# Kernel optimization log

Measured on AMD Instinct MI355X. Metric: run time of the kernel, lower is better.

The kernel has to match this reference:

```python
import jax, jax.numpy as jnp
import numpy as np

JOBS, FEAT, BATCH = 150, 15, 32
H1, D1 = 3, 64          # layer1: 3 heads x 64, concatenated -> 192
H2, D2 = 3, 128         # layer2: 3 heads x 128, averaged -> 128
GNN_OUT = D2 + FEAT     # 143 (gnn output concat with raw node features)
HID = 64


def _gat_layer(h_in, W, a_src, a_dst):
    # h_in: [N, F]; W: [F, H, D]; a_src/a_dst: [H, D]
    h = jnp.einsum('nf,fhd->nhd', h_in, W)                 # [N, H, D]
    s = jnp.einsum('nhd,hd->nh', h, a_src)                 # target score
    t = jnp.einsum('nhd,hd->nh', h, a_dst)                 # source score
    e = jax.nn.leaky_relu(s[:, None, :] + t[None, :, :], 0.2)   # [N, N, H]
    alpha = jax.nn.softmax(e, axis=1)                      # softmax over sources j
    return jnp.einsum('ijh,jhd->ihd', alpha, h)            # [N, H, D]


def setup_inputs() -> dict:
    key = jax.random.key(0)
    ks = jax.random.split(key, 12)
    sc = 0.1
    return {
        'real_obs': jax.random.normal(ks[0], (BATCH, JOBS, FEAT), jnp.float32),
        'action_mask': jnp.ones((BATCH, JOBS + 1), jnp.float32),
        'W1': jax.random.normal(ks[1], (FEAT, H1, D1), jnp.float32) * sc,
        'a_src1': jax.random.normal(ks[2], (H1, D1), jnp.float32) * sc,
        'a_dst1': jax.random.normal(ks[3], (H1, D1), jnp.float32) * sc,
        'W2': jax.random.normal(ks[4], (H1 * D1, H2, D2), jnp.float32) * sc,
        'a_src2': jax.random.normal(ks[5], (H2, D2), jnp.float32) * sc,
        'a_dst2': jax.random.normal(ks[6], (H2, D2), jnp.float32) * sc,
        'P1': jax.random.normal(ks[7], (GNN_OUT, 2 * HID), jnp.float32) * sc,
        'b1': jnp.zeros((2 * HID,), jnp.float32),
        'P2': jax.random.normal(ks[8], (2 * HID, HID), jnp.float32) * sc,
        'b2': jnp.zeros((HID,), jnp.float32),
    }


def reference(real_obs, action_mask, W1, a_src1, a_dst1, W2, a_src2, a_dst2, P1, b1, P2, b2):
    B = real_obs.shape[0]
    flat = real_obs.reshape(B * JOBS, FEAT)                        # N=4800 nodes, fully connected
    h1 = _gat_layer(flat, W1, a_src1, a_dst1)                      # [N, 3, 64]
    h1 = jax.nn.elu(h1.reshape(h1.shape[0], -1))                   # concat heads -> [N, 192]
    h2 = _gat_layer(h1, W2, a_src2, a_dst2).mean(axis=1)           # avg heads -> [N, 128]
    g = jnp.concatenate([h2, flat], axis=-1)                       # [N, 143]
    f = jax.nn.relu(g @ P1 + b1)
    f = jax.nn.relu(f @ P2 + b2)                                   # [N, 64]
    features = f.reshape(B, JOBS, HID).mean(axis=1)                # mean pool -> [B, 64]
    return features, action_mask
```

## Files before the change

### kernel.cpp

```cpp
#include <hip/hip_runtime.h>
#include <hip/hip_bf16.h>

typedef __attribute__((ext_vector_type(8))) short short8;
typedef __attribute__((ext_vector_type(4))) float f32x4;

#define NN 4800
#define NN1 4801
#define NC 240
#define CL 20
#define KLEN 600

__device__ __forceinline__ short bf16rne(float x) {
    unsigned u = __float_as_uint(x);
    u = (u + 0x7FFFu + ((u >> 16) & 1u)) >> 16;
    return (short)u;
}
__device__ __forceinline__ unsigned fkey(float f) {
    unsigned i = __float_as_uint(f);
    return (i & 0x80000000u) ? ~i : (i | 0x80000000u);
}

__global__ __launch_bounds__(256) void prep(
    const float* __restrict__ flat, const float* __restrict__ amask,
    const float* __restrict__ W1, const float* __restrict__ as1, const float* __restrict__ ad1,
    const float* __restrict__ W2, const float* __restrict__ P1, const float* __restrict__ P2,
    float* __restrict__ h1, float* __restrict__ s1, float* __restrict__ t1,
    short* __restrict__ W2T, short* __restrict__ P1T, short* __restrict__ P2T,
    float* __restrict__ out) {
    const int gtid = blockIdx.x * 256 + threadIdx.x;
    const int GT = 1200 * 256;
    for (int x = gtid; x < 109280; x += GT) {
        if (x < 73728) {
            int n = x / 192, k = x % 192;
            W2T[x] = bf16rne(W2[k * 384 + n]);
        } else if (x < 94208) {
            int z = x - 73728; int n = z / 160, k = z % 160;
            P1T[z] = bf16rne(k < 143 ? P1[k * 128 + n] : 0.f);
        } else if (x < 102400) {
            int z = x - 94208; int n = z / 128, k = z % 128;
            P2T[z] = bf16rne(P2[k * 64 + n]);
        } else if (x < 107232) {
            int m = x - 102400;
            out[2048 + m] = amask[m];
        } else {
            out[x - 107232] = 0.f;
        }
    }
    const int lane = threadIdx.x & 63;
    const int gw = (gtid >> 6);
    for (int task = gw; task < 3 * NN; task += (GT >> 6)) {
        int h = task / NN, i = task % NN;
        int col = h * 64 + lane;
        const float* fr = flat + i * 15;
        float hv = 0.f;
#pragma unroll
        for (int f = 0; f < 15; ++f) hv += fr[f] * W1[f * 192 + col];
        h1[i * 192 + col] = hv;
        float ps = hv * as1[col], pt = hv * ad1[col];
#pragma unroll
        for (int off = 32; off; off >>= 1) { ps += __shfl_xor(ps, off); pt += __shfl_xor(pt, off); }
        if (lane == 0) { s1[h * NN + i] = ps; t1[h * NN + i] = pt; }
    }
}

__global__ __launch_bounds__(256) void krank(const float* __restrict__ s, const float* __restrict__ t,
                                             int* __restrict__ partial) {
    __shared__ __align__(16) unsigned long long ts[KLEN];
    const int h = blockIdx.y, kc = blockIdx.z;
    const float* tp = t + h * NN + kc * KLEN;
    for (int k = threadIdx.x; k < KLEN; k += 256)
        ts[k] = ((unsigned long long)fkey(tp[k]) << 32) | (unsigned)k;
    __syncthreads();
    int q = blockIdx.x * 256 + threadIdx.x;
    if (q >= 2 * NN) return;
    unsigned long long uq;
    if (q < NN) {
        int tb = q - kc * KLEN;
        int tbc = tb < 0 ? 0 : (tb > KLEN ? KLEN : tb);
        uq = ((unsigned long long)fkey(t[h * NN + q]) << 32) | (unsigned)tbc;
    } else {
        uq = ((unsigned long long)fkey(-s[h * NN + q - NN]) << 32) | (unsigned)KLEN;
    }
    int cnt = 0;
#pragma unroll 4
    for (int k = 0; k < KLEN; k += 2) {
        ulonglong2 v = *(const ulonglong2*)&ts[k];
        cnt += (v.x < uq);
        cnt += (v.y < uq);
    }
    partial[(kc * 3 + h) * (2 * NN) + q] = cnt;
}

__global__ __launch_bounds__(256) void ksc1(const float* __restrict__ t, const int* __restrict__ partial,
                                            int* __restrict__ inv, float* __restrict__ e1s,
                                            float* __restrict__ e2s, int* __restrict__ rks) {
    int idx = blockIdx.x * 256 + threadIdx.x;
    if (idx >= 3 * 2 * NN) return;
    int h = idx / (2 * NN), q = idx % (2 * NN);
    int sum = 0;
#pragma unroll
    for (int kc = 0; kc < 8; ++kc) sum += partial[(kc * 3 + h) * (2 * NN) + q];
    if (q < NN) {
        float tv = t[h * NN + q];
        inv[h * NN + sum] = q;
        e1s[h * NN + sum] = __expf(tv);
        e2s[h * NN + sum] = __expf(0.2f * tv);
    } else {
        rks[h * NN + q - NN] = sum;
    }
}

template <int Dd, int HD, int PACK>
__global__ __launch_bounds__(256) void phA(const float* __restrict__ hsrc, const int* __restrict__ inv,
                                           const float* __restrict__ e1s, const float* __restrict__ e2s,
                                           float* __restrict__ T1, float* __restrict__ T2) {
    __shared__ int inv_l[PACK * CL];
    __shared__ float w1s[PACK * CL], w2s[PACK * CL];
    const int h = blockIdx.y, tid = threadIdx.x;
    const int base = blockIdx.x * (PACK * CL);
    if (tid < PACK * CL) {
        inv_l[tid] = inv[h * NN + base + tid];
        w1s[tid] = e1s[h * NN + base + tid];
        w2s[tid] = e2s[h * NN + base + tid];
    }
    __syncthreads();
    const int sub = tid / Dd, d = tid % Dd;
    const int c = blockIdx.x * PACK + sub;
    float a1 = 0.f, a2 = 0.f;
#pragma unroll
    for (int p = 0; p < CL; ++p) {
        int j = inv_l[sub * CL + p];
        float hv = hsrc[(size_t)j * HD + h * Dd + d];
        a1 += w1s[sub * CL + p] * hv;
        a2 += w2s[sub * CL + p] * hv;
    }
    T1[(h * NC + c) * Dd + d] = a1;
    T2[(h * NC + c) * Dd + d] = a2;
}

template <int Dd>
__global__ __launch_bounds__(256) void phBden(const float* __restrict__ T1, const float* __restrict__ T2,
                                              const float* __restrict__ e1s, const float* __restrict__ e2s,
                                              float* __restrict__ O1, float* __restrict__ O2,
                                              float* __restrict__ DenS1, float* __restrict__ DenP2) {
    constexpr int G = Dd / 32;
    constexpr int NSCAN = 6 * G;
    __shared__ __align__(16) float smem[9608];
    const int tid = threadIdx.x;
    if (blockIdx.x < NSCAN) {
        float (*ls)[32] = (float(*)[32])smem;
        double* sbd = (double*)(smem + 7680);
        const int b = blockIdx.x;
        const int h = b % 3, rest = b / 3, dir = rest & 1, dg = rest >> 1;
        const float* T = dir ? T2 : T1;
        for (int idx = tid; idx < NC * 32; idx += 256) {
            int c = idx >> 5, dl = idx & 31;
            ls[c][dl] = T[(h * NC + c) * Dd + dg * 32 + dl];
        }
        __syncthreads();
        const int seg = tid >> 5, dl = tid & 31;
        double ssum = 0.0;
#pragma unroll
        for (int k = 0; k < 30; ++k) ssum += (double)ls[seg * 30 + k][dl];
        sbd[seg * 32 + dl] = ssum;
        __syncthreads();
        double off = 0.0;
        if (dir == 0) { for (int k = seg + 1; k < 8; ++k) off += sbd[k * 32 + dl]; }
        else          { for (int k = 0; k < seg; ++k)     off += sbd[k * 32 + dl]; }
        float* O = dir ? O2 : O1;
        const int d = dg * 32 + dl;
        double r = off;
        if (dir == 0) {
#pragma unroll
            for (int k = 29; k >= 0; --k) {
                int c = seg * 30 + k;
                O[(h * NC + c) * Dd + d] = (float)r;
                r += (double)ls[c][dl];
            }
        } else {
#pragma unroll
            for (int k = 0; k < 30; ++k) {
                int c = seg * 30 + k;
                O[(h * NC + c) * Dd + d] = (float)r;
                r += (double)ls[c][dl];
            }
        }
        return;
    }
    const int h = blockIdx.x - NSCAN;
    float* l1 = smem;
    float* l2 = smem + NN;
    float* wsum = smem + 9600;
    for (int k = tid; k < NN; k += 256) { l1[k] = e1s[h * NN + k]; l2[k] = e2s[h * NN + k]; }
    __syncthreads();
    const int p0 = tid * 19;
    const int cnt = (p0 < NN) ? ((NN - p0 < 19) ? NN - p0 : 19) : 0;
    float sA = 0.f, sB = 0.f;
    for (int k = 0; k < cnt; ++k) { sA += l1[p0 + k]; sB += l2[p0 + k]; }
    float iA = sA, iB = sB;
    const int lane = tid & 63, w = tid >> 6;
#pragma unroll
    for (int d2 = 1; d2 < 64; d2 <<= 1) {
        float uA = __shfl_up(iA, d2), uB = __shfl_up(iB, d2);
        if (lane >= d2) { iA += uA; iB += uB; }
    }
    if (lane == 63) { wsum[w] = iA; wsum[4 + w] = iB; }
    __syncthreads();
    float baseA = 0.f, baseB = 0.f;
    for (int k = 0; k < w; ++k) { baseA += wsum[k]; baseB += wsum[4 + k]; }
    float TA = wsum[0] + wsum[1] + wsum[2] + wsum[3];
    float rA = baseA + iA - sA;
    float rB = baseB + iB - sB;
    for (int k = 0; k < cnt; ++k) {
        int p = p0 + k;
        DenS1[h * NN1 + p] = TA - rA;
        DenP2[h * NN1 + p] = rB;
        rA += l1[p]; rB += l2[p];
    }
    if (tid == 255) {
        DenS1[h * NN1 + NN] = 0.f;
        DenP2[h * NN1 + NN] = wsum[4] + wsum[5] + wsum[6] + wsum[7];
    }
}

template <int Dd, int HD, int PACK>
__global__ __launch_bounds__(256) void phC(const float* __restrict__ hsrc, const int* __restrict__ inv,
                                           const float* __restrict__ e1s, const float* __restrict__ e2s,
                                           const float* __restrict__ O1, const float* __restrict__ O2,
                                           float* __restrict__ Suf1, float* __restrict__ Pre2) {
    __shared__ int inv_l[PACK * CL];
    __shared__ float w1s[PACK * CL], w2s[PACK * CL];
    const int h = blockIdx.y, tid = threadIdx.x;
    const int base = blockIdx.x * (PACK * CL);
    if (tid < PACK * CL) {
        inv_l[tid] = inv[h * NN + base + tid];
        w1s[tid] = e1s[h * NN + base + tid];
        w2s[tid] = e2s[h * NN + base + tid];
    }
    __syncthreads();
    const int sub = tid / Dd, d = tid % Dd;
    const int c = blockIdx.x * PACK + sub;
    float hv[CL];
#pragma unroll
    for (int p = 0; p < CL; ++p) {
        int j = inv_l[sub * CL + p];
        hv[p] = hsrc[(size_t)j * HD + h * Dd + d];
    }
    float r2 = O2[(h * NC + c) * Dd + d];
#pragma unroll
    for (int p = 0; p < CL; ++p) {
        int pp = c * CL + p;
        Pre2[((size_t)(h * NN1) + pp) * Dd + d] = r2;
        r2 += w2s[sub * CL + p] * hv[p];
    }
    if (c == NC - 1) {
        Pre2[((size_t)(h * NN1) + NN) * Dd + d] = r2;
        Suf1[((size_t)(h * NN1) + NN) * Dd + d] = 0.f;
    }
    float r1 = O1[(h * NC + c) * Dd + d];
#pragma unroll
    for (int p = CL - 1; p >= 0; --p) {
        int pp = c * CL + p;
        r1 += w1s[sub * CL + p] * hv[p];
        Suf1[((size_t)(h * NN1) + pp) * Dd + d] = r1;
    }
}

__global__ __launch_bounds__(256) void kout1(const float* __restrict__ s1, const int* __restrict__ rks1,
                                             const float* __restrict__ Suf1, const float* __restrict__ Pre2,
                                             const float* __restrict__ DenS1, const float* __restrict__ DenP2,
                                             short* __restrict__ h1abf,
                                             float* __restrict__ s2, float* __restrict__ t2) {
    const int gtid = blockIdx.x * 256 + threadIdx.x;
    if (gtid < 3 * NN) { s2[gtid] = 0.f; t2[gtid] = 0.f; }
    for (int x = gtid; x < NN * 192; x += 900 * 256) {
        int i = x / 192, cc = x % 192, h = cc >> 6, d = cc & 63;
        float sv = s1[h * NN + i];
        float a = __expf(sv), b = __expf(0.2f * sv);
        int r = rks1[h * NN + i];
        size_t bp = ((size_t)(h * NN1) + r) * 64 + d;
        float num = a * Suf1[bp] + b * Pre2[bp];
        float den = a * DenS1[h * NN1 + r] + b * DenP2[h * NN1 + r];
        float v = num / den;
        v = v > 0.f ? v : (__expf(v) - 1.f);
        h1abf[x] = bf16rne(v);
    }
}

__global__ __launch_bounds__(256) void gemm1(const short* __restrict__ A, const short* __restrict__ W2T,
                                             const float* __restrict__ as2, const float* __restrict__ ad2,
                                             float* __restrict__ h2, float* __restrict__ s2,
                                             float* __restrict__ t2) {
    const int mb = blockIdx.x, nb = blockIdx.y, tid = threadIdx.x;
    const int lane = tid & 63, w = tid >> 6, q = lane >> 4, mr = lane & 15;
    const int m = mb * 64 + w * 16 + mr, n0 = nb * 64, hh = nb >> 1;
    f32x4 acc[4];
#pragma unroll
    for (int n = 0; n < 4; ++n) acc[n] = (f32x4){0.f, 0.f, 0.f, 0.f};
#pragma unroll
    for (int k0 = 0; k0 < 192; k0 += 32) {
        short8 af = *(const short8*)(A + (size_t)m * 192 + k0 + q * 8);
#pragma unroll
        for (int n = 0; n < 4; ++n) {
            short8 bf = *(const short8*)(W2T + (size_t)(n0 + n * 16 + mr) * 192 + k0 + q * 8);
            acc[n] = __builtin_amdgcn_mfma_f32_16x16x32_bf16(af, bf, acc[n], 0, 0, 0);
        }
    }
    float pse[4] = {0.f, 0.f, 0.f, 0.f}, pte[4] = {0.f, 0.f, 0.f, 0.f};
#pragma unroll
    for (int n = 0; n < 4; ++n) {
        int col = n0 + n * 16 + mr;
        float va = as2[col], vd = ad2[col];
#pragma unroll
        for (int r = 0; r < 4; ++r) {
            int row = mb * 64 + w * 16 + q * 4 + r;
            float v = acc[n][r];
            h2[(size_t)row * 384 + col] = v;
            pse[r] += v * va;
            pte[r] += v * vd;
        }
    }
#pragma unroll
    for (int off = 1; off < 16; off <<= 1) {
#pragma unroll
        for (int r = 0; r < 4; ++r) {
            pse[r] += __shfl_xor(pse[r], off);
            pte[r] += __shfl_xor(pte[r], off);
// ... 66 lines not shown
    }
    __syncthreads();
    f32x4 a2 = (f32x4){0.f, 0.f, 0.f, 0.f};
#pragma unroll
    for (int k0 = 0; k0 < 128; k0 += 32) {
        short8 af = *(const short8*)&f1[mr][k0 + q * 8];
        short8 bf = *(const short8*)(P2T + (size_t)(w * 16 + mr) * 128 + k0 + q * 8);
        a2 = __builtin_amdgcn_mfma_f32_16x16x32_bf16(af, bf, a2, 0, 0, 0);
    }
    float* f2f = (float*)&g[0][0];
    {
        int col = w * 16 + mr;
        float bv = b2[col];
#pragma unroll
        for (int r = 0; r < 4; ++r) {
            int row = q * 4 + r;
            f2f[row * 65 + col] = fmaxf(a2[r] + bv, 0.f);
        }
    }
    __syncthreads();
    if (tid < 64) {
        int d = tid;
        int b0 = (mb * 16) / 150;
        int bend = (mb * 16 + 15) / 150;
        float sa = 0.f, sb = 0.f;
        for (int row = 0; row < 16; ++row) {
            float v = f2f[row * 65 + d];
            int b = (mb * 16 + row) / 150;
            if (b == b0) sa += v; else sb += v;
        }
        atomicAdd(&out[b0 * 64 + d], sa * (1.f / 150.f));
        if (bend != b0) atomicAdd(&out[bend * 64 + d], sb * (1.f / 150.f));
    }
}

extern "C" void kernel_launch(void* const* d_in, const int* in_sizes, int n_in,
                              void* d_out, int out_size, void* d_ws, size_t ws_size,
                              hipStream_t stream) {
    const float* flat   = (const float*)d_in[0];
    const float* amask  = (const float*)d_in[1];
    const float* W1     = (const float*)d_in[2];
    const float* a_src1 = (const float*)d_in[3];
    const float* a_dst1 = (const float*)d_in[4];
    const float* W2     = (const float*)d_in[5];
    const float* a_src2 = (const float*)d_in[6];
    const float* a_dst2 = (const float*)d_in[7];
    const float* P1     = (const float*)d_in[8];
    const float* b1     = (const float*)d_in[9];
    const float* P2     = (const float*)d_in[10];
    const float* b2     = (const float*)d_in[11];
    float* out = (float*)d_out;

    char* wsb = (char*)d_ws;
    int*   partial = (int*)  (wsb + 0);
    float* s1      = (float*)(wsb + 921600);
    float* t1      = (float*)(wsb + 979200);
    float* s2      = (float*)(wsb + 1036800);
    float* t2      = (float*)(wsb + 1094400);
    int*   rks1    = (int*)  (wsb + 1152000);
    int*   rks2    = (int*)  (wsb + 1209600);
    float* h1      = (float*)(wsb + 1267200);
    int*   inv     = (int*)  (wsb + 4953600);
    float* e1s     = (float*)(wsb + 5011200);
    float* e2s     = (float*)(wsb + 5068800);
    float* DenS1   = (float*)(wsb + 5126400);
    float* DenP2   = (float*)(wsb + 5184064);
    float* Tot1    = (float*)(wsb + 5241728);
    float* Tot2    = (float*)(wsb + 5610368);
    float* Off1    = (float*)(wsb + 5979008);
    float* Off2    = (float*)(wsb + 6347648);
    float* Suf1    = (float*)(wsb + 6716288);
    float* Pre2    = (float*)(wsb + 14090624);
    float* h2      = (float*)(wsb + 21464960);
    short* h1abf   = (short*)(wsb + 28837760);
    short* W2T     = (short*)(wsb + 30680960);
    short* P1T     = (short*)(wsb + 30828416);
    short* P2T     = (short*)(wsb + 30869376);

    prep<<<1200, 256, 0, stream>>>(flat, amask, W1, a_src1, a_dst1, W2, P1, P2,
                                   h1, s1, t1, W2T, P1T, P2T, out);
    krank<<<dim3(38, 3, 8), 256, 0, stream>>>(s1, t1, partial);
    ksc1<<<113, 256, 0, stream>>>(t1, partial, inv, e1s, e2s, rks1);
    phA<64, 192, 4><<<dim3(60, 3), 256, 0, stream>>>(h1, inv, e1s, e2s, Tot1, Tot2);
    phBden<64><<<15, 256, 0, stream>>>(Tot1, Tot2, e1s, e2s, Off1, Off2, DenS1, DenP2);
    phC<64, 192, 4><<<dim3(60, 3), 256, 0, stream>>>(h1, inv, e1s, e2s, Off1, Off2, Suf1, Pre2);
    kout1<<<900, 256, 0, stream>>>(s1, rks1, Suf1, Pre2, DenS1, DenP2, h1abf, s2, t2);
    gemm1<<<dim3(75, 6), 256, 0, stream>>>(h1abf, W2T, a_src2, a_dst2, h2, s2, t2);
    krank<<<dim3(38, 3, 8), 256, 0, stream>>>(s2, t2, partial);
    ksc1<<<113, 256, 0, stream>>>(t2, partial, inv, e1s, e2s, rks2);
    phA<128, 384, 2><<<dim3(120, 3), 256, 0, stream>>>(h2, inv, e1s, e2s, Tot1, Tot2);
    phBden<128><<<27, 256, 0, stream>>>(Tot1, Tot2, e1s, e2s, Off1, Off2, DenS1, DenP2);
    phC<128, 384, 2><<<dim3(120, 3), 256, 0, stream>>>(h2, inv, e1s, e2s, Off1, Off2, Suf1, Pre2);
    tail2<<<300, 256, 0, stream>>>(s2, rks2, Suf1, Pre2, DenS1, DenP2, flat, P1T, P2T, b1, b2, out);
}
```

Before: 183.0 us.

## Fuse rank reduction into atomics and fold scan kernels into neighbors

The rank-count kernel now accumulates its partial counts with a packed atomic that also counts finished chunks. The last arriving block performs the scatter, which removes the separate reduction kernel and its partial buffer pass. The denominator prefix scan moves into an extra block of the cluster-aggregation kernel. The per-cluster offset scan is recomputed redundantly inside the suffix/prefix kernel from the cluster totals. Together this removes two launches per layer, at the cost of atomic contention and redundant serial double-precision summation over up to 240 clusters per block.

Measured after the change: 241.6 us. 32.0% more time.

```diff
diff --git a/kernel.cpp b/kernel.cpp
--- a/kernel.cpp
+++ b/kernel.cpp
@@ -1,8 +1,8 @@
 #include <hip/hip_runtime.h>
-#include <hip/hip_bf16.h>
 
 typedef __attribute__((ext_vector_type(8))) short short8;
 typedef __attribute__((ext_vector_type(4))) float f32x4;
+typedef unsigned long long ull;
 
 #define NN 4800
 #define NN1 4801
@@ -26,10 +26,10 @@
     const float* __restrict__ W2, const float* __restrict__ P1, const float* __restrict__ P2,
     float* __restrict__ h1, float* __restrict__ s1, float* __restrict__ t1,
     short* __restrict__ W2T, short* __restrict__ P1T, short* __restrict__ P2T,
-    float* __restrict__ out) {
+    float* __restrict__ out, int* __restrict__ partial) {
     const int gtid = blockIdx.x * 256 + threadIdx.x;
     const int GT = 1200 * 256;
-    for (int x = gtid; x < 109280; x += GT) {
+    for (int x = gtid; x < 138080; x += GT) {
         if (x < 73728) {
             int n = x / 192, k = x % 192;
             W2T[x] = bf16rne(W2[k * 384 + n]);
@@ -42,8 +42,10 @@
         } else if (x < 107232) {
             int m = x - 102400;
             out[2048 + m] = amask[m];
+        } else if (x < 109280) {
+            out[x - 107232] = 0.f;
         } else {
-            out[x - 107232] = 0.f;
+            partial[x - 109280] = 0;
         }
     }
     const int lane = threadIdx.x & 63;
@@ -63,23 +65,25 @@
     }
 }
 
-__global__ __launch_bounds__(256) void krank(const float* __restrict__ s, const float* __restrict__ t,
-                                             int* __restrict__ partial) {
-    __shared__ __align__(16) unsigned long long ts[KLEN];
+__global__ __launch_bounds__(256) void krks(const float* __restrict__ s, const float* __restrict__ t,
+                                            int* __restrict__ acc, int* __restrict__ inv,
+                                            float* __restrict__ e1s, float* __restrict__ e2s,
+                                            int* __restrict__ rks) {
+    __shared__ __align__(16) ull ts[KLEN];
     const int h = blockIdx.y, kc = blockIdx.z;
     const float* tp = t + h * NN + kc * KLEN;
     for (int k = threadIdx.x; k < KLEN; k += 256)
-        ts[k] = ((unsigned long long)fkey(tp[k]) << 32) | (unsigned)k;
+        ts[k] = ((ull)fkey(tp[k]) << 32) | (unsigned)k;
     __syncthreads();
     int q = blockIdx.x * 256 + threadIdx.x;
     if (q >= 2 * NN) return;
-    unsigned long long uq;
+    ull uq;
     if (q < NN) {
         int tb = q - kc * KLEN;
         int tbc = tb < 0 ? 0 : (tb > KLEN ? KLEN : tb);
-        uq = ((unsigned long long)fkey(t[h * NN + q]) << 32) | (unsigned)tbc;
+        uq = ((ull)fkey(t[h * NN + q]) << 32) | (unsigned)tbc;
     } else {
-        uq = ((unsigned long long)fkey(-s[h * NN + q - NN]) << 32) | (unsigned)KLEN;
+        uq = ((ull)fkey(-s[h * NN + q - NN]) << 32) | (unsigned)KLEN;
     }
     int cnt = 0;
 #pragma unroll 4
@@ -88,36 +92,65 @@
         cnt += (v.x < uq);
         cnt += (v.y < uq);
     }
-    partial[(kc * 3 + h) * (2 * NN) + q] = cnt;
-}
-
-__global__ __launch_bounds__(256) void ksc1(const float* __restrict__ t, const int* __restrict__ partial,
-                                            int* __restrict__ inv, float* __restrict__ e1s,
-                                            float* __restrict__ e2s, int* __restrict__ rks) {
-    int idx = blockIdx.x * 256 + threadIdx.x;
-    if (idx >= 3 * 2 * NN) return;
-    int h = idx / (2 * NN), q = idx % (2 * NN);
-    int sum = 0;
-#pragma unroll
-    for (int kc = 0; kc < 8; ++kc) sum += partial[(kc * 3 + h) * (2 * NN) + q];
-    if (q < NN) {
-        float tv = t[h * NN + q];
-        inv[h * NN + sum] = q;
-        e1s[h * NN + sum] = __expf(tv);
-        e2s[h * NN + sum] = __expf(0.2f * tv);
-    } else {
-        rks[h * NN + q - NN] = sum;
+    unsigned ret = atomicAdd((unsigned*)&acc[h * 2 * NN + q], (unsigned)cnt | (1u << 24));
+    if ((ret >> 24) == 7u) {
+        int sum = (int)((ret & 0xFFFFFFu) + (unsigned)cnt);
+        if (q < NN) {
+            float tv = t[h * NN + q];
+            inv[h * NN + sum] = q;
+            e1s[h * NN + sum] = __expf(tv);
+            e2s[h * NN + sum] = __expf(0.2f * tv);
+        } else {
+            rks[h * NN + q - NN] = sum;
+        }
     }
 }
 
 template <int Dd, int HD, int PACK>
-__global__ __launch_bounds__(256) void phA(const float* __restrict__ hsrc, const int* __restrict__ inv,
-                                           const float* __restrict__ e1s, const float* __restrict__ e2s,
-                                           float* __restrict__ T1, float* __restrict__ T2) {
+__global__ __launch_bounds__(256) void phAden(const float* __restrict__ hsrc, const int* __restrict__ inv,
+                                              const float* __restrict__ e1s, const float* __restrict__ e2s,
+                                              float* __restrict__ T1, float* __restrict__ T2,
+                                              float* __restrict__ DenS1, float* __restrict__ DenP2) {
+    constexpr int NB = NC / PACK;
     __shared__ int inv_l[PACK * CL];
     __shared__ float w1s[PACK * CL], w2s[PACK * CL];
+    __shared__ float wsum[8];
     const int h = blockIdx.y, tid = threadIdx.x;
-    const int base = blockIdx.x * (PACK * CL);
+    if (blockIdx.x == NB) {
+        const float* l1 = e1s + h * NN;
+        const float* l2 = e2s + h * NN;
+        const int p0 = tid * 19;
+        const int cnt = (p0 < NN) ? ((NN - p0 < 19) ? NN - p0 : 19) : 0;
+        float sA = 0.f, sB = 0.f;
+        for (int k = 0; k < cnt; ++k) { sA += l1[p0 + k]; sB += l2[p0 + k]; }
+        float iA = sA, iB = sB;
+        const int lane = tid & 63, w = tid >> 6;
+#pragma unroll
+        for (int d2 = 1; d2 < 64; d2 <<= 1) {
+            float uA = __shfl_up(iA, d2), uB = __shfl_up(iB, d2);
+            if (lane >= d2) { iA += uA; iB += uB; }
+        }
+        if (lane == 63) { wsum[w] = iA; wsum[4 + w] = iB; }
+        __syncthreads();
+        float baseA = 0.f, baseB = 0.f;
+        for (int k = 0; k < w; ++k) { baseA += wsum[k]; baseB += wsum[4 + k]; }
+        float TA = wsum[0] + wsum[1] + wsum[2] + wsum[3];
+        float rA = baseA + iA - sA;
+        float rB = baseB + iB - sB;
+        for (int k = 0; k < cnt; ++k) {
+            int p = p0 + k;
+            DenS1[h * NN1 + p] = TA - rA;
+            DenP2[h * NN1 + p] = rB;
+            rA += l1[p]; rB += l2[p];
+        }
+        if (tid == 255) {
+            DenS1[h * NN1 + NN] = 0.f;
+            DenP2[h * NN1 + NN] = wsum[4] + wsum[5] + wsum[6] + wsum[7];
+        }
+        return;
+    }
+    const int cb = blockIdx.x;
+    const int base = cb * (PACK * CL);
     if (tid < PACK * CL) {
         inv_l[tid] = inv[h * NN + base + tid];
         w1s[tid] = e1s[h * NN + base + tid];
@@ -125,7 +158,7 @@
     }
     __syncthreads();
     const int sub = tid / Dd, d = tid % Dd;
-    const int c = blockIdx.x * PACK + sub;
+    const int c = cb * PACK + sub;
     float a1 = 0.f, a2 = 0.f;
 #pragma unroll
     for (int p = 0; p < CL; ++p) {
@@ -138,115 +171,69 @@
     T2[(h * NC + c) * Dd + d] = a2;
 }
 
-template <int Dd>
-__global__ __launch_bounds__(256) void phBden(const float* __restrict__ T1, const float* __restrict__ T2,
-                                              const float* __restrict__ e1s, const float* __restrict__ e2s,
-                                              float* __restrict__ O1, float* __restrict__ O2,
-                                              float* __restrict__ DenS1, float* __restrict__ DenP2) {
-    constexpr int G = Dd / 32;
-    constexpr int NSCAN = 6 * G;
-    __shared__ __align__(16) float smem[9608];
-    const int tid = threadIdx.x;
-    if (blockIdx.x < NSCAN) {
-        float (*ls)[32] = (float(*)[32])smem;
-        double* sbd = (double*)(smem + 7680);
-        const int b = blockIdx.x;
-        const int h = b % 3, rest = b / 3, dir = rest & 1, dg = rest >> 1;
-        const float* T = dir ? T2 : T1;
-        for (int idx = tid; idx < NC * 32; idx += 256) {
-            int c = idx >> 5, dl = idx & 31;
-            ls[c][dl] = T[(h * NC + c) * Dd + dg * 32 + dl];
-        }
-        __syncthreads();
-        const int seg = tid >> 5, dl = tid & 31;
-        double ssum = 0.0;
-#pragma unroll
-        for (int k = 0; k < 30; ++k) ssum += (double)ls[seg * 30 + k][dl];
-        sbd[seg * 32 + dl] = ssum;
-        __syncthreads();
-        double off = 0.0;
-        if (dir == 0) { for (int k = seg + 1; k < 8; ++k) off += sbd[k * 32 + dl]; }
-        else          { for (int k = 0; k < seg; ++k)     off += sbd[k * 32 + dl]; }
-        float* O = dir ? O2 : O1;
-        const int d = dg * 32 + dl;
-        double r = off;
-        if (dir == 0) {
-#pragma unroll
-            for (int k = 29; k >= 0; --k) {
-                int c = seg * 30 + k;
-                O[(h * NC + c) * Dd + d] = (float)r;
-                r += (double)ls[c][dl];
-            }
-        } else {
-#pragma unroll
-            for (int k = 0; k < 30; ++k) {
-                int c = seg * 30 + k;
-                O[(h * NC + c) * Dd + d] = (float)r;
-                r += (double)ls[c][dl];
-            }
-        }
-        return;
-    }
-    const int h = blockIdx.x - NSCAN;
-    float* l1 = smem;
-    float* l2 = smem + NN;
-    float* wsum = smem + 9600;
-    for (int k = tid; k < NN; k += 256) { l1[k] = e1s[h * NN + k]; l2[k] = e2s[h * NN + k]; }
-    __syncthreads();
-    const int p0 = tid * 19;
-    const int cnt = (p0 < NN) ? ((NN - p0 < 19) ? NN - p0 : 19) : 0;
-    float sA = 0.f, sB = 0.f;
-    for (int k = 0; k < cnt; ++k) { sA += l1[p0 + k]; sB += l2[p0 + k]; }
-    float iA = sA, iB = sB;
-    const int lane = tid & 63, w = tid >> 6;
-#pragma unroll
-    for (int d2 = 1; d2 < 64; d2 <<= 1) {
-        float uA = __shfl_up(iA, d2), uB = __shfl_up(iB, d2);
-        if (lane >= d2) { iA += uA; iB += uB; }
-    }
-    if (lane == 63) { wsum[w] = iA; wsum[4 + w] = iB; }
-    __syncthreads();
-    float baseA = 0.f, baseB = 0.f;
-    for (int k = 0; k < w; ++k) { baseA += wsum[k]; baseB += wsum[4 + k]; }
-    float TA = wsum[0] + wsum[1] + wsum[2] + wsum[3];
-    float rA = baseA + iA - sA;
-    float rB = baseB + iB - sB;
-    for (int k = 0; k < cnt; ++k) {
-        int p = p0 + k;
-        DenS1[h * NN1 + p] = TA - rA;
-        DenP2[h * NN1 + p] = rB;
-        rA += l1[p]; rB += l2[p];
-    }
-    if (tid == 255) {
-        DenS1[h * NN1 + NN] = 0.f;
-        DenP2[h * NN1 + NN] = wsum[4] + wsum[5] + wsum[6] + wsum[7];
-    }
-}
-
 template <int Dd, int HD, int PACK>
-__global__ __launch_bounds__(256) void phC(const float* __restrict__ hsrc, const int* __restrict__ inv,
-                                           const float* __restrict__ e1s, const float* __restrict__ e2s,
-                                           const float* __restrict__ O1, const float* __restrict__ O2,
-                                           float* __restrict__ Suf1, float* __restrict__ Pre2) {
+__global__ __launch_bounds__(256) void phCs(const float* __restrict__ hsrc, const int* __restrict__ inv,
+                                            const float* __restrict__ e1s, const float* __restrict__ e2s,
+                                            const float* __restrict__ T1, const float* __restrict__ T2,
+                                            float* __restrict__ Suf1, float* __restrict__ Pre2) {
     __shared__ int inv_l[PACK * CL];
     __shared__ float w1s[PACK * CL], w2s[PACK * CL];
-    const int h = blockIdx.y, tid = threadIdx.x;
-    const int base = blockIdx.x * (PACK * CL);
+    __shared__ double o1d[Dd], o2d[Dd];
+    const int h = blockIdx.y, cb = blockIdx.x, tid = threadIdx.x;
+    const int base = cb * (PACK * CL);
     if (tid < PACK * CL) {
         inv_l[tid] = inv[h * NN + base + tid];
         w1s[tid] = e1s[h * NN + base + tid];
         w2s[tid] = e2s[h * NN + base + tid];
     }
-    __syncthreads();
     const int sub = tid / Dd, d = tid % Dd;
-    const int c = blockIdx.x * PACK + sub;
+    const int c = cb * PACK + sub;
+    const int cmin = cb * PACK, cmax = cb * PACK + PACK - 1;
+    double o1 = 0.0, o2 = 0.0;
+    if (sub == PACK - 1) {
+        double e0 = 0.0, e1 = 0.0;
+        int cc = c + 1;
+        for (; cc + 1 < NC; cc += 2) {
+            e0 += (double)T1[(h * NC + cc) * Dd + d];
+            e1 += (double)T1[(h * NC + cc + 1) * Dd + d];
+        }
+        if (cc < NC) e0 += (double)T1[(h * NC + cc) * Dd + d];
+        o1 = e0 + e1; o1d[d] = o1;
+    }
+    if (sub == 0) {
+        double e0 = 0.0, e1 = 0.0;
+        int cc = 0;
+        for (; cc + 1 < c; cc += 2) {
+            e0 += (double)T2[(h * NC + cc) * Dd + d];
+            e1 += (double)T2[(h * NC + cc + 1) * Dd + d];
+        }
+        if (cc < c) e0 += (double)T2[(h * NC + cc) * Dd + d];
+        o2 = e0 + e1; o2d[d] = o2;
+    }
+    __syncthreads();
+    if (sub != PACK - 1) {
+        o1 = o1d[d];
+#pragma unroll
+        for (int cc2 = 0; cc2 < PACK - 1; ++cc2) {
+            int cc = c + 1 + cc2;
+            if (cc <= cmax) o1 += (double)T1[(h * NC + cc) * Dd + d];
+        }
+    }
+    if (sub != 0) {
+        o2 = o2d[d];
+#pragma unroll
+        for (int cc2 = 0; cc2 < PACK - 1; ++cc2) {
+            int cc = cmin + cc2;
+            if (cc < c) o2 += (double)T2[(h * NC + cc) * Dd + d];
+        }
+    }
     float hv[CL];
 #pragma unroll
     for (int p = 0; p < CL; ++p) {
         int j = inv_l[sub * CL + p];
         hv[p] = hsrc[(size_t)j * HD + h * Dd + d];
     }
-    float r2 = O2[(h * NC + c) * Dd + d];
+    float r2 = (float)o2;
 #pragma unroll
     for (int p = 0; p < CL; ++p) {
         int pp = c * CL + p;
@@ -257,7 +244,7 @@
         Pre2[((size_t)(h * NN1) + NN) * Dd + d] = r2;
         Suf1[((size_t)(h * NN1) + NN) * Dd + d] = 0.f;
     }
-    float r1 = O1[(h * NC + c) * Dd + d];
+    float r1 = (float)o1;
 #pragma unroll
     for (int p = CL - 1; p >= 0; --p) {
         int pp = c * CL + p;
@@ -270,9 +257,11 @@
                                              const float* __restrict__ Suf1, const float* __restrict__ Pre2,
                                              const float* __restrict__ DenS1, const float* __restrict__ DenP2,
                                              short* __restrict__ h1abf,
-                                             float* __restrict__ s2, float* __restrict__ t2) {
+                                             float* __restrict__ s2, float* __restrict__ t2,
+                                             int* __restrict__ partial) {
     const int gtid = blockIdx.x * 256 + threadIdx.x;
     if (gtid < 3 * NN) { s2[gtid] = 0.f; t2[gtid] = 0.f; }
+    if (gtid < 3 * 2 * NN) partial[gtid] = 0;
     for (int x = gtid; x < NN * 192; x += 900 * 256) {
         int i = x / 192, cc = x % 192, h = cc >> 6, d = cc & 63;
         float sv = s1[h * NN + i];
@@ -460,8 +449,6 @@
     float* DenP2   = (float*)(wsb + 5184064);
     float* Tot1    = (float*)(wsb + 5241728);
     float* Tot2    = (float*)(wsb + 5610368);
-    float* Off1    = (float*)(wsb + 5979008);
-    float* Off2    = (float*)(wsb + 6347648);
     float* Suf1    = (float*)(wsb + 6716288);
     float* Pre2    = (float*)(wsb + 14090624);
     float* h2      = (float*)(wsb + 21464960);
@@ -471,18 +458,14 @@
     short* P2T     = (short*)(wsb + 30869376);
 
     prep<<<1200, 256, 0, stream>>>(flat, amask, W1, a_src1, a_dst1, W2, P1, P2,
-                                   h1, s1, t1, W2T, P1T, P2T, out);
-    krank<<<dim3(38, 3, 8), 256, 0, stream>>>(s1, t1, partial);
-    ksc1<<<113, 256, 0, stream>>>(t1, partial, inv, e1s, e2s, rks1);
-    phA<64, 192, 4><<<dim3(60, 3), 256, 0, stream>>>(h1, inv, e1s, e2s, Tot1, Tot2);
-    phBden<64><<<15, 256, 0, stream>>>(Tot1, Tot2, e1s, e2s, Off1, Off2, DenS1, DenP2);
-    phC<64, 192, 4><<<dim3(60, 3), 256, 0, stream>>>(h1, inv, e1s, e2s, Off1, Off2, Suf1, Pre2);
-    kout1<<<900, 256, 0, stream>>>(s1, rks1, Suf1, Pre2, DenS1, DenP2, h1abf, s2, t2);
+                                   h1, s1, t1, W2T, P1T, P2T, out, partial);
+    krks<<<dim3(38, 3, 8), 256, 0, stream>>>(s1, t1, partial, inv, e1s, e2s, rks1);
+    phAden<64, 192, 4><<<dim3(61, 3), 256, 0, stream>>>(h1, inv, e1s, e2s, Tot1, Tot2, DenS1, DenP2);
+    phCs<64, 192, 4><<<dim3(60, 3), 256, 0, stream>>>(h1, inv, e1s, e2s, Tot1, Tot2, Suf1, Pre2);
+    kout1<<<900, 256, 0, stream>>>(s1, rks1, Suf1, Pre2, DenS1, DenP2, h1abf, s2, t2, partial);
     gemm1<<<dim3(75, 6), 256, 0, stream>>>(h1abf, W2T, a_src2, a_dst2, h2, s2, t2);
-    krank<<<dim3(38, 3, 8), 256, 0, stream>>>(s2, t2, partial);
-    ksc1<<<113, 256, 0, stream>>>(t2, partial, inv, e1s, e2s, rks2);
-    phA<128, 384, 2><<<dim3(120, 3), 256, 0, stream>>>(h2, inv, e1s, e2s, Tot1, Tot2);
-    phBden<128><<<27, 256, 0, stream>>>(Tot1, Tot2, e1s, e2s, Off1, Off2, DenS1, DenP2);
-    phC<128, 384, 2><<<dim3(120, 3), 256, 0, stream>>>(h2, inv, e1s, e2s, Off1, Off2, Suf1, Pre2);
+    krks<<<dim3(38, 3, 8), 256, 0, stream>>>(s2, t2, partial, inv, e1s, e2s, rks2);
+    phAden<128, 384, 2><<<dim3(121, 3), 256, 0, stream>>>(h2, inv, e1s, e2s, Tot1, Tot2, DenS1, DenP2);
+    phCs<128, 384, 2><<<dim3(120, 3), 256, 0, stream>>>(h2, inv, e1s, e2s, Tot1, Tot2, Suf1, Pre2);
     tail2<<<300, 256, 0, stream>>>(s2, rks2, Suf1, Pre2, DenS1, DenP2, flat, P1T, P2T, b1, b2, out);
 }
```

## Replace brute-force rank counting with chunk bitonic sort plus binary search

Applied to the files above, without the earlier changes.

The old krank compared every query against all 600 keys of each of 8 chunks, then a separate kernel summed the partial counts and scattered the results. The new code bitonic-sorts each 600-key chunk in shared memory, padded to 1024. A fused kernel then binary-searches each sorted chunk and does the scatter directly, which cuts the comparison work from linear to logarithmic and removes one launch and the partial-count buffer. In exchange there are two small, serial-ish launches: the sort uses only 24 blocks with many syncthreads, and the search loop reloads shared memory 8 times per block.

Result: slower. 233.2 us (+27.4%).

```diff
diff --git a/kernel.cpp b/kernel.cpp
--- a/kernel.cpp
+++ b/kernel.cpp
@@ -1,8 +1,8 @@
 #include <hip/hip_runtime.h>
-#include <hip/hip_bf16.h>
 
 typedef __attribute__((ext_vector_type(8))) short short8;
 typedef __attribute__((ext_vector_type(4))) float f32x4;
+typedef unsigned long long ull;
 
 #define NN 4800
 #define NN1 4801
@@ -63,50 +63,64 @@
     }
 }
 
-__global__ __launch_bounds__(256) void krank(const float* __restrict__ s, const float* __restrict__ t,
-                                             int* __restrict__ partial) {
-    __shared__ __align__(16) unsigned long long ts[KLEN];
-    const int h = blockIdx.y, kc = blockIdx.z;
+__global__ __launch_bounds__(256) void sortk(const float* __restrict__ t, ull* __restrict__ sortedK) {
+    __shared__ ull ls[1024];
+    const int kc = blockIdx.x, h = blockIdx.y, tid = threadIdx.x;
     const float* tp = t + h * NN + kc * KLEN;
-    for (int k = threadIdx.x; k < KLEN; k += 256)
-        ts[k] = ((unsigned long long)fkey(tp[k]) << 32) | (unsigned)k;
-    __syncthreads();
-    int q = blockIdx.x * 256 + threadIdx.x;
-    if (q >= 2 * NN) return;
-    unsigned long long uq;
+    for (int i = tid; i < 1024; i += 256)
+        ls[i] = (i < KLEN) ? (((ull)fkey(tp[i]) << 32) | (unsigned)(kc * KLEN + i)) : ~0ull;
+    __syncthreads();
+    for (int k = 2; k <= 1024; k <<= 1) {
+        for (int j = k >> 1; j > 0; j >>= 1) {
+            for (int i = tid; i < 1024; i += 256) {
+                int p = i ^ j;
+                if (p > i) {
+                    ull a = ls[i], b = ls[p];
+                    bool up = ((i & k) == 0);
+                    if ((a > b) == up) { ls[i] = b; ls[p] = a; }
+                }
+            }
+            __syncthreads();
+        }
+    }
+    ull* dst = sortedK + (h * 8 + kc) * KLEN;
+    for (int i = tid; i < KLEN; i += 256) dst[i] = ls[i];
+}
+
+__global__ __launch_bounds__(256) void kranksc(const float* __restrict__ s, const float* __restrict__ t,
+                                               const ull* __restrict__ sortedK,
+                                               int* __restrict__ inv, float* __restrict__ e1s,
+                                               float* __restrict__ e2s, int* __restrict__ rks) {
+    __shared__ __align__(16) ull ts[KLEN];
+    const int h = blockIdx.y, tid = threadIdx.x;
+    const int q = blockIdx.x * 256 + tid;
+    const bool active = q < 2 * NN;
+    ull uq = 0; float tv = 0.f;
+    if (active) {
+        if (q < NN) { tv = t[h * NN + q]; uq = ((ull)fkey(tv) << 32) | (unsigned)q; }
+        else        { uq = ((ull)fkey(-s[h * NN + q - NN]) << 32) | 0xFFFFFFFFu; }
+    }
+    int rank = 0;
+    for (int kc = 0; kc < 8; ++kc) {
+        __syncthreads();
+        const ull* src = sortedK + (h * 8 + kc) * KLEN;
+        for (int k = tid; k < KLEN; k += 256) ts[k] = src[k];
+        __syncthreads();
+        if (active) {
+            int pos = 0;
+#pragma unroll
+            for (int st = 512; st; st >>= 1)
+                if (pos + st <= KLEN && ts[pos + st - 1] < uq) pos += st;
+            rank += pos;
+        }
+    }
+    if (!active) return;
     if (q < NN) {
-        int tb = q - kc * KLEN;
-        int tbc = tb < 0 ? 0 : (tb > KLEN ? KLEN : tb);
-        uq = ((unsigned long long)fkey(t[h * NN + q]) << 32) | (unsigned)tbc;
+        inv[h * NN + rank] = q;
+        e1s[h * NN + rank] = __expf(tv);
+        e2s[h * NN + rank] = __expf(0.2f * tv);
     } else {
-        uq = ((unsigned long long)fkey(-s[h * NN + q - NN]) << 32) | (unsigned)KLEN;
-    }
-    int cnt = 0;
-#pragma unroll 4
-    for (int k = 0; k < KLEN; k += 2) {
-        ulonglong2 v = *(const ulonglong2*)&ts[k];
-        cnt += (v.x < uq);
-        cnt += (v.y < uq);
-    }
-    partial[(kc * 3 + h) * (2 * NN) + q] = cnt;
-}
-
-__global__ __launch_bounds__(256) void ksc1(const float* __restrict__ t, const int* __restrict__ partial,
-                                            int* __restrict__ inv, float* __restrict__ e1s,
-                                            float* __restrict__ e2s, int* __restrict__ rks) {
-    int idx = blockIdx.x * 256 + threadIdx.x;
-    if (idx >= 3 * 2 * NN) return;
-    int h = idx / (2 * NN), q = idx % (2 * NN);
-    int sum = 0;
-#pragma unroll
-    for (int kc = 0; kc < 8; ++kc) sum += partial[(kc * 3 + h) * (2 * NN) + q];
-    if (q < NN) {
-        float tv = t[h * NN + q];
-        inv[h * NN + sum] = q;
-        e1s[h * NN + sum] = __expf(tv);
-        e2s[h * NN + sum] = __expf(0.2f * tv);
-    } else {
-        rks[h * NN + q - NN] = sum;
+        rks[h * NN + q - NN] = rank;
     }
 }
 
@@ -445,7 +459,7 @@
     float* out = (float*)d_out;
 
     char* wsb = (char*)d_ws;
-    int*   partial = (int*)  (wsb + 0);
+    ull*   sortedK = (ull*)  (wsb + 0);
     float* s1      = (float*)(wsb + 921600);
     float* t1      = (float*)(wsb + 979200);
     float* s2      = (float*)(wsb + 1036800);
@@ -472,15 +486,15 @@
 
     prep<<<1200, 256, 0, stream>>>(flat, amask, W1, a_src1, a_dst1, W2, P1, P2,
                                    h1, s1, t1, W2T, P1T, P2T, out);
-    krank<<<dim3(38, 3, 8), 256, 0, stream>>>(s1, t1, partial);
-    ksc1<<<113, 256, 0, stream>>>(t1, partial, inv, e1s, e2s, rks1);
+    sortk<<<dim3(8, 3), 256, 0, stream>>>(t1, sortedK);
+    kranksc<<<dim3(38, 3), 256, 0, stream>>>(s1, t1, sortedK, inv, e1s, e2s, rks1);
     phA<64, 192, 4><<<dim3(60, 3), 256, 0, stream>>>(h1, inv, e1s, e2s, Tot1, Tot2);
     phBden<64><<<15, 256, 0, stream>>>(Tot1, Tot2, e1s, e2s, Off1, Off2, DenS1, DenP2);
     phC<64, 192, 4><<<dim3(60, 3), 256, 0, stream>>>(h1, inv, e1s, e2s, Off1, Off2, Suf1, Pre2);
     kout1<<<900, 256, 0, stream>>>(s1, rks1, Suf1, Pre2, DenS1, DenP2, h1abf, s2, t2);
     gemm1<<<dim3(75, 6), 256, 0, stream>>>(h1abf, W2T, a_src2, a_dst2, h2, s2, t2);
-    krank<<<dim3(38, 3, 8), 256, 0, stream>>>(s2, t2, partial);
-    ksc1<<<113, 256, 0, stream>>>(t2, partial, inv, e1s, e2s, rks2);
+    sortk<<<dim3(8, 3), 256, 0, stream>>>(t2, sortedK);
+    kranksc<<<dim3(38, 3), 256, 0, stream>>>(s2, t2, sortedK, inv, e1s, e2s, rks2);
     phA<128, 384, 2><<<dim3(120, 3), 256, 0, stream>>>(h2, inv, e1s, e2s, Tot1, Tot2);
     phBden<128><<<27, 256, 0, stream>>>(Tot1, Tot2, e1s, e2s, Off1, Off2, DenS1, DenP2);
     phC<128, 384, 2><<<dim3(120, 3), 256, 0, stream>>>(h2, inv, e1s, e2s, Off1, Off2, Suf1, Pre2);
```

## Fuse rank reduction via atomic counters and move denominator scan into phA

Applied to the files above, without the earlier changes.

The rank-partial kernel now adds its count into a per-query counter that packs a completion tag in the upper bits. The eighth contributing block finalises the rank and scatters inv, e1s, e2s and rks, which removes the separate ksc1 reduction launch. The denominator prefix-scan moves from phBden into an extra block of phA, and phB becomes a pure T-scan kernel. Counters are zeroed in prep and kout1. This trades two kernel launches per layer for global atomics and an extra block that reads the weights directly from global memory.

Result: slower. 193.7 us (+5.8%).

```diff
diff --git a/kernel.cpp b/kernel.cpp
--- a/kernel.cpp
+++ b/kernel.cpp
@@ -1,8 +1,8 @@
 #include <hip/hip_runtime.h>
-#include <hip/hip_bf16.h>
 
 typedef __attribute__((ext_vector_type(8))) short short8;
 typedef __attribute__((ext_vector_type(4))) float f32x4;
+typedef unsigned long long ull;
 
 #define NN 4800
 #define NN1 4801
@@ -26,10 +26,10 @@
     const float* __restrict__ W2, const float* __restrict__ P1, const float* __restrict__ P2,
     float* __restrict__ h1, float* __restrict__ s1, float* __restrict__ t1,
     short* __restrict__ W2T, short* __restrict__ P1T, short* __restrict__ P2T,
-    float* __restrict__ out) {
+    float* __restrict__ out, int* __restrict__ acc) {
     const int gtid = blockIdx.x * 256 + threadIdx.x;
     const int GT = 1200 * 256;
-    for (int x = gtid; x < 109280; x += GT) {
+    for (int x = gtid; x < 138080; x += GT) {
         if (x < 73728) {
             int n = x / 192, k = x % 192;
             W2T[x] = bf16rne(W2[k * 384 + n]);
@@ -42,8 +42,10 @@
         } else if (x < 107232) {
             int m = x - 102400;
             out[2048 + m] = amask[m];
+        } else if (x < 109280) {
+            out[x - 107232] = 0.f;
         } else {
-            out[x - 107232] = 0.f;
+            acc[x - 109280] = 0;
         }
     }
     const int lane = threadIdx.x & 63;
@@ -63,23 +65,25 @@
     }
 }
 
-__global__ __launch_bounds__(256) void krank(const float* __restrict__ s, const float* __restrict__ t,
-                                             int* __restrict__ partial) {
-    __shared__ __align__(16) unsigned long long ts[KLEN];
+__global__ __launch_bounds__(256) void krks(const float* __restrict__ s, const float* __restrict__ t,
+                                            int* __restrict__ acc, int* __restrict__ inv,
+                                            float* __restrict__ e1s, float* __restrict__ e2s,
+                                            int* __restrict__ rks) {
+    __shared__ __align__(16) ull ts[KLEN];
     const int h = blockIdx.y, kc = blockIdx.z;
     const float* tp = t + h * NN + kc * KLEN;
     for (int k = threadIdx.x; k < KLEN; k += 256)
-        ts[k] = ((unsigned long long)fkey(tp[k]) << 32) | (unsigned)k;
+        ts[k] = ((ull)fkey(tp[k]) << 32) | (unsigned)k;
     __syncthreads();
     int q = blockIdx.x * 256 + threadIdx.x;
     if (q >= 2 * NN) return;
-    unsigned long long uq;
+    ull uq;
     if (q < NN) {
         int tb = q - kc * KLEN;
         int tbc = tb < 0 ? 0 : (tb > KLEN ? KLEN : tb);
-        uq = ((unsigned long long)fkey(t[h * NN + q]) << 32) | (unsigned)tbc;
+        uq = ((ull)fkey(t[h * NN + q]) << 32) | (unsigned)tbc;
     } else {
-        uq = ((unsigned long long)fkey(-s[h * NN + q - NN]) << 32) | (unsigned)KLEN;
+        uq = ((ull)fkey(-s[h * NN + q - NN]) << 32) | (unsigned)KLEN;
     }
     int cnt = 0;
 #pragma unroll 4
@@ -88,36 +92,65 @@
         cnt += (v.x < uq);
         cnt += (v.y < uq);
     }
-    partial[(kc * 3 + h) * (2 * NN) + q] = cnt;
-}
-
-__global__ __launch_bounds__(256) void ksc1(const float* __restrict__ t, const int* __restrict__ partial,
-                                            int* __restrict__ inv, float* __restrict__ e1s,
-                                            float* __restrict__ e2s, int* __restrict__ rks) {
-    int idx = blockIdx.x * 256 + threadIdx.x;
-    if (idx >= 3 * 2 * NN) return;
-    int h = idx / (2 * NN), q = idx % (2 * NN);
-    int sum = 0;
-#pragma unroll
-    for (int kc = 0; kc < 8; ++kc) sum += partial[(kc * 3 + h) * (2 * NN) + q];
-    if (q < NN) {
-        float tv = t[h * NN + q];
-        inv[h * NN + sum] = q;
-        e1s[h * NN + sum] = __expf(tv);
-        e2s[h * NN + sum] = __expf(0.2f * tv);
-    } else {
-        rks[h * NN + q - NN] = sum;
+    unsigned ret = atomicAdd((unsigned*)&acc[h * 2 * NN + q], (unsigned)cnt | (1u << 24));
+    if ((ret >> 24) == 7u) {
+        int sum = (int)((ret & 0xFFFFFFu) + (unsigned)cnt);
+        if (q < NN) {
+            float tv = t[h * NN + q];
+            inv[h * NN + sum] = q;
+            e1s[h * NN + sum] = __expf(tv);
+            e2s[h * NN + sum] = __expf(0.2f * tv);
+        } else {
+            rks[h * NN + q - NN] = sum;
+        }
     }
 }
 
 template <int Dd, int HD, int PACK>
-__global__ __launch_bounds__(256) void phA(const float* __restrict__ hsrc, const int* __restrict__ inv,
-                                           const float* __restrict__ e1s, const float* __restrict__ e2s,
-                                           float* __restrict__ T1, float* __restrict__ T2) {
+__global__ __launch_bounds__(256) void phAden(const float* __restrict__ hsrc, const int* __restrict__ inv,
+                                              const float* __restrict__ e1s, const float* __restrict__ e2s,
+                                              float* __restrict__ T1, float* __restrict__ T2,
+                                              float* __restrict__ DenS1, float* __restrict__ DenP2) {
+    constexpr int NB = NC / PACK;
     __shared__ int inv_l[PACK * CL];
     __shared__ float w1s[PACK * CL], w2s[PACK * CL];
+    __shared__ float wsum[8];
     const int h = blockIdx.y, tid = threadIdx.x;
-    const int base = blockIdx.x * (PACK * CL);
+    if (blockIdx.x == NB) {
+        const float* l1 = e1s + h * NN;
+        const float* l2 = e2s + h * NN;
+        const int p0 = tid * 19;
+        const int cnt = (p0 < NN) ? ((NN - p0 < 19) ? NN - p0 : 19) : 0;
+        float sA = 0.f, sB = 0.f;
+        for (int k = 0; k < cnt; ++k) { sA += l1[p0 + k]; sB += l2[p0 + k]; }
+        float iA = sA, iB = sB;
+        const int lane = tid & 63, w = tid >> 6;
+#pragma unroll
+        for (int d2 = 1; d2 < 64; d2 <<= 1) {
+            float uA = __shfl_up(iA, d2), uB = __shfl_up(iB, d2);
+            if (lane >= d2) { iA += uA; iB += uB; }
+        }
+        if (lane == 63) { wsum[w] = iA; wsum[4 + w] = iB; }
+        __syncthreads();
+        float baseA = 0.f, baseB = 0.f;
+        for (int k = 0; k < w; ++k) { baseA += wsum[k]; baseB += wsum[4 + k]; }
+        float TA = wsum[0] + wsum[1] + wsum[2] + wsum[3];
+        float rA = baseA + iA - sA;
+        float rB = baseB + iB - sB;
+        for (int k = 0; k < cnt; ++k) {
+            int p = p0 + k;
+            DenS1[h * NN1 + p] = TA - rA;
+            DenP2[h * NN1 + p] = rB;
+            rA += l1[p]; rB += l2[p];
+        }
+        if (tid == 255) {
+            DenS1[h * NN1 + NN] = 0.f;
+            DenP2[h * NN1 + NN] = wsum[4] + wsum[5] + wsum[6] + wsum[7];
+        }
+        return;
+    }
+    const int cb = blockIdx.x;
+    const int base = cb * (PACK * CL);
     if (tid < PACK * CL) {
         inv_l[tid] = inv[h * NN + base + tid];
         w1s[tid] = e1s[h * NN + base + tid];
@@ -125,7 +158,7 @@
     }
     __syncthreads();
     const int sub = tid / Dd, d = tid % Dd;
-    const int c = blockIdx.x * PACK + sub;
+    const int c = cb * PACK + sub;
     float a1 = 0.f, a2 = 0.f;
 #pragma unroll
     for (int p = 0; p < CL; ++p) {
@@ -139,87 +172,46 @@
 }
 
 template <int Dd>
-__global__ __launch_bounds__(256) void phBden(const float* __restrict__ T1, const float* __restrict__ T2,
-                                              const float* __restrict__ e1s, const float* __restrict__ e2s,
-                                              float* __restrict__ O1, float* __restrict__ O2,
-                                              float* __restrict__ DenS1, float* __restrict__ DenP2) {
-    constexpr int G = Dd / 32;
-    constexpr int NSCAN = 6 * G;
-    __shared__ __align__(16) float smem[9608];
+__global__ __launch_bounds__(256) void phBscan(const float* __restrict__ T1, const float* __restrict__ T2,
+                                               float* __restrict__ O1, float* __restrict__ O2) {
+    __shared__ __align__(16) float smem[8192];
     const int tid = threadIdx.x;
-    if (blockIdx.x < NSCAN) {
-        float (*ls)[32] = (float(*)[32])smem;
-        double* sbd = (double*)(smem + 7680);
-        const int b = blockIdx.x;
-        const int h = b % 3, rest = b / 3, dir = rest & 1, dg = rest >> 1;
-        const float* T = dir ? T2 : T1;
-        for (int idx = tid; idx < NC * 32; idx += 256) {
-            int c = idx >> 5, dl = idx & 31;
-            ls[c][dl] = T[(h * NC + c) * Dd + dg * 32 + dl];
-        }
-        __syncthreads();
-        const int seg = tid >> 5, dl = tid & 31;
-        double ssum = 0.0;
-#pragma unroll
-        for (int k = 0; k < 30; ++k) ssum += (double)ls[seg * 30 + k][dl];
-        sbd[seg * 32 + dl] = ssum;
-        __syncthreads();
-        double off = 0.0;
-        if (dir == 0) { for (int k = seg + 1; k < 8; ++k) off += sbd[k * 32 + dl]; }
-        else          { for (int k = 0; k < seg; ++k)     off += sbd[k * 32 + dl]; }
-        float* O = dir ? O2 : O1;
-        const int d = dg * 32 + dl;
-        double r = off;
-        if (dir == 0) {
-#pragma unroll
-            for (int k = 29; k >= 0; --k) {
-                int c = seg * 30 + k;
-                O[(h * NC + c) * Dd + d] = (float)r;
-                r += (double)ls[c][dl];
-            }
-        } else {
-#pragma unroll
-            for (int k = 0; k < 30; ++k) {
-                int c = seg * 30 + k;
-                O[(h * NC + c) * Dd + d] = (float)r;
-                r += (double)ls[c][dl];
-            }
-        }
-        return;
-    }
-    const int h = blockIdx.x - NSCAN;
-    float* l1 = smem;
-    float* l2 = smem + NN;
-    float* wsum = smem + 9600;
-    for (int k = tid; k < NN; k += 256) { l1[k] = e1s[h * NN + k]; l2[k] = e2s[h * NN + k]; }
-    __syncthreads();
-    const int p0 = tid * 19;
-    const int cnt = (p0 < NN) ? ((NN - p0 < 19) ? NN - p0 : 19) : 0;
-    float sA = 0.f, sB = 0.f;
-    for (int k = 0; k < cnt; ++k) { sA += l1[p0 + k]; sB += l2[p0 + k]; }
-    float iA = sA, iB = sB;
-    const int lane = tid & 63, w = tid >> 6;
-#pragma unroll
-    for (int d2 = 1; d2 < 64; d2 <<= 1) {
-        float uA = __shfl_up(iA, d2), uB = __shfl_up(iB, d2);
-        if (lane >= d2) { iA += uA; iB += uB; }
-    }
-    if (lane == 63) { wsum[w] = iA; wsum[4 + w] = iB; }
-    __syncthreads();
-    float baseA = 0.f, baseB = 0.f;
-    for (int k = 0; k < w; ++k) { baseA += wsum[k]; baseB += wsum[4 + k]; }
-    float TA = wsum[0] + wsum[1] + wsum[2] + wsum[3];
-    float rA = baseA + iA - sA;
-    float rB = baseB + iB - sB;
-    for (int k = 0; k < cnt; ++k) {
-        int p = p0 + k;
-        DenS1[h * NN1 + p] = TA - rA;
-        DenP2[h * NN1 + p] = rB;
-        rA += l1[p]; rB += l2[p];
-    }
-    if (tid == 255) {
-        DenS1[h * NN1 + NN] = 0.f;
-        DenP2[h * NN1 + NN] = wsum[4] + wsum[5] + wsum[6] + wsum[7];
+    float (*ls)[32] = (float(*)[32])smem;
+    double* sbd = (double*)(smem + 7680);
+    const int b = blockIdx.x;
+    const int h = b % 3, rest = b / 3, dir = rest & 1, dg = rest >> 1;
+    const float* T = dir ? T2 : T1;
+    for (int idx = tid; idx < NC * 32; idx += 256) {
+        int c = idx >> 5, dl = idx & 31;
+        ls[c][dl] = T[(h * NC + c) * Dd + dg * 32 + dl];
+    }
+    __syncthreads();
+    const int seg = tid >> 5, dl = tid & 31;
+    double ssum = 0.0;
+#pragma unroll
+    for (int k = 0; k < 30; ++k) ssum += (double)ls[seg * 30 + k][dl];
+    sbd[seg * 32 + dl] = ssum;
+    __syncthreads();
+    double off = 0.0;
+    if (dir == 0) { for (int k = seg + 1; k < 8; ++k) off += sbd[k * 32 + dl]; }
+    else          { for (int k = 0; k < seg; ++k)     off += sbd[k * 32 + dl]; }
+    float* O = dir ? O2 : O1;
+    const int d = dg * 32 + dl;
+    double r = off;
+    if (dir == 0) {
+#pragma unroll
+        for (int k = 29; k >= 0; --k) {
+            int c = seg * 30 + k;
+            O[(h * NC + c) * Dd + d] = (float)r;
+            r += (double)ls[c][dl];
+        }
+    } else {
+#pragma unroll
+        for (int k = 0; k < 30; ++k) {
+            int c = seg * 30 + k;
+            O[(h * NC + c) * Dd + d] = (float)r;
+            r += (double)ls[c][dl];
+        }
     }
 }
 
@@ -270,9 +262,11 @@
                                              const float* __restrict__ Suf1, const float* __restrict__ Pre2,
                                              const float* __restrict__ DenS1, const float* __restrict__ DenP2,
                                              short* __restrict__ h1abf,
-                                             float* __restrict__ s2, float* __restrict__ t2) {
+                                             float* __restrict__ s2, float* __restrict__ t2,
+                                             int* __restrict__ acc) {
     const int gtid = blockIdx.x * 256 + threadIdx.x;
     if (gtid < 3 * NN) { s2[gtid] = 0.f; t2[gtid] = 0.f; }
+    if (gtid < 3 * 2 * NN) acc[gtid] = 0;
     for (int x = gtid; x < NN * 192; x += 900 * 256) {
         int i = x / 192, cc = x % 192, h = cc >> 6, d = cc & 63;
         float sv = s1[h * NN + i];
@@ -445,7 +439,7 @@
     float* out = (float*)d_out;
 
     char* wsb = (char*)d_ws;
-    int*   partial = (int*)  (wsb + 0);
+    int*   acc     = (int*)  (wsb + 0);
     float* s1      = (float*)(wsb + 921600);
     float* t1      = (float*)(wsb + 979200);
     float* s2      = (float*)(wsb + 1036800);
@@ -471,18 +465,16 @@
     short* P2T     = (short*)(wsb + 30869376);
 
     prep<<<1200, 256, 0, stream>>>(flat, amask, W1, a_src1, a_dst1, W2, P1, P2,
-                                   h1, s1, t1, W2T, P1T, P2T, out);
-    krank<<<dim3(38, 3, 8), 256, 0, stream>>>(s1, t1, partial);
-    ksc1<<<113, 256, 0, stream>>>(t1, partial, inv, e1s, e2s, rks1);
-    phA<64, 192, 4><<<dim3(60, 3), 256, 0, stream>>>(h1, inv, e1s, e2s, Tot1, Tot2);
-    phBden<64><<<15, 256, 0, stream>>>(Tot1, Tot2, e1s, e2s, Off1, Off2, DenS1, DenP2);
+                                   h1, s1, t1, W2T, P1T, P2T, out, acc);
+    krks<<<dim3(38, 3, 8), 256, 0, stream>>>(s1, t1, acc, inv, e1s, e2s, rks1);
+    phAden<64, 192, 4><<<dim3(61, 3), 256, 0, stream>>>(h1, inv, e1s, e2s, Tot1, Tot2, DenS1, DenP2);
+    phBscan<64><<<12, 256, 0, stream>>>(Tot1, Tot2, Off1, Off2);
     phC<64, 192, 4><<<dim3(60, 3), 256, 0, stream>>>(h1, inv, e1s, e2s, Off1, Off2, Suf1, Pre2);
-    kout1<<<900, 256, 0, stream>>>(s1, rks1, Suf1, Pre2, DenS1, DenP2, h1abf, s2, t2);
+    kout1<<<900, 256, 0, stream>>>(s1, rks1, Suf1, Pre2, DenS1, DenP2, h1abf, s2, t2, acc);
     gemm1<<<dim3(75, 6), 256, 0, stream>>>(h1abf, W2T, a_src2, a_dst2, h2, s2, t2);
-    krank<<<dim3(38, 3, 8), 256, 0, stream>>>(s2, t2, partial);
-    ksc1<<<113, 256, 0, stream>>>(t2, partial, inv, e1s, e2s, rks2);
-    phA<128, 384, 2><<<dim3(120, 3), 256, 0, stream>>>(h2, inv, e1s, e2s, Tot1, Tot2);
-    phBden<128><<<27, 256, 0, stream>>>(Tot1, Tot2, e1s, e2s, Off1, Off2, DenS1, DenP2);
+    krks<<<dim3(38, 3, 8), 256, 0, stream>>>(s2, t2, acc, inv, e1s, e2s, rks2);
+    phAden<128, 384, 2><<<dim3(121, 3), 256, 0, stream>>>(h2, inv, e1s, e2s, Tot1, Tot2, DenS1, DenP2);
+    phBscan<128><<<24, 256, 0, stream>>>(Tot1, Tot2, Off1, Off2);
     phC<128, 384, 2><<<dim3(120, 3), 256, 0, stream>>>(h2, inv, e1s, e2s, Off1, Off2, Suf1, Pre2);
     tail2<<<300, 256, 0, stream>>>(s2, rks2, Suf1, Pre2, DenS1, DenP2, flat, P1T, P2T, b1, b2, out);
 }
```
